# Kernel optimization log

Measured on AMD Instinct MI355X. Metric: run time of the kernel, lower is better.

Reference implementation:

```python
import jax, jax.numpy as jnp
import numpy as np

BN_EPS = 1e-5


def setup_inputs() -> dict:
    key = jax.random.key(0)
    ks = jax.random.split(key, 13)
    B, Ct, H, W = 2, 64, 32, 32
    Co, E = 32, 64
    Ho, Wo = 3 * H, 3 * W
    s = 0.05
    return {
        "x_thermal": jax.random.normal(ks[0], (B, Ct, H, W), jnp.float32),
        "x_optical": jax.random.normal(ks[1], (B, Co, Ho, Wo), jnp.float32),
        # 1x1 conv weights stored as [out_c, in_c]
        "q_w": jax.random.normal(ks[2], (E, Ct), jnp.float32) * s,
        "q_b": jax.random.normal(ks[3], (E,), jnp.float32) * s,
        "k_w": jax.random.normal(ks[4], (E, Co), jnp.float32) * s,
        "k_b": jax.random.normal(ks[5], (E,), jnp.float32) * s,
        "v_w": jax.random.normal(ks[6], (Co, Co), jnp.float32) * s,
        "v_b": jax.random.normal(ks[7], (Co,), jnp.float32) * s,
        # out ConvBlock: 1x1 conv (no bias) -> BatchNorm (eval, running stats) -> ReLU
        "out_w": jax.random.normal(ks[8], (Ct, Co), jnp.float32) * s,
        "bn_gamma": jnp.ones((Ct,), jnp.float32) + jax.random.normal(ks[9], (Ct,), jnp.float32) * 0.01,
        "bn_beta": jax.random.normal(ks[10], (Ct,), jnp.float32) * 0.01,
        "bn_mean": jax.random.normal(ks[11], (Ct,), jnp.float32) * 0.01,
        "bn_var": jax.random.uniform(ks[12], (Ct,), jnp.float32, 0.5, 1.5),
    }


def reference(x_thermal, x_optical, q_w, q_b, k_w, k_b, v_w, v_b,
              out_w, bn_gamma, bn_beta, bn_mean, bn_var):
    B, Co, Ho, Wo = x_optical.shape
    N = Ho * Wo
    # F.interpolate(mode='bilinear', align_corners=False) == jax.image.resize 'bilinear' (half-pixel)
    x_up = jax.image.resize(x_thermal, (B, x_thermal.shape[1], Ho, Wo), method="bilinear")
    # 1x1 conv projections
    q = (jnp.einsum("bchw,ec->behw", x_up, q_w) + q_b[None, :, None, None]).reshape(B, -1, N)
    k = (jnp.einsum("bchw,ec->behw", x_optical, k_w) + k_b[None, :, None, None]).reshape(B, -1, N)
    v = (jnp.einsum("bchw,oc->bohw", x_optical, v_w) + v_b[None, :, None, None]).reshape(B, -1, N)
    E = q.shape[1]
    # attn[b, n, m] = sum_e q[b,e,n] * k[b,e,m]  (full N x N score matrix)
    scores = jnp.einsum("ben,bem->bnm", q, k) / jnp.sqrt(jnp.asarray(E, q.dtype))
    attn = jax.nn.softmax(scores, axis=-1)
    # out = v @ attn^T : out[b,o,n] = sum_m v[b,o,m] * attn[b,n,m]
    out = jnp.einsum("bom,bnm->bon", v, attn).reshape(B, Co, Ho, Wo)
    # out ConvBlock: 1x1 conv (bias=False) -> BatchNorm (eval) -> ReLU
    g = jnp.einsum("bchw,tc->bthw", out, out_w)
    g = (g - bn_mean[None, :, None, None]) * (bn_gamma / jnp.sqrt(bn_var + BN_EPS))[None, :, None, None] \
        + bn_beta[None, :, None, None]
    return jax.nn.relu(g)
```

## Files before the change

kernel.cpp:

```cpp
#include <hip/hip_runtime.h>
#include <hip/hip_bf16.h>


constexpr int B   = 2;
constexpr int N   = 9216;
constexpr int E   = 64;
constexpr int CO  = 32;
constexpr int CT  = 64;
constexpr int KVBLK = 64;

constexpr int KP_BLK = 288;
constexpr int VP_BLK = 288;
constexpr int QP_BLK = 32;

typedef _Float16 f16x8 __attribute__((ext_vector_type(8)));
typedef _Float16 f16x4 __attribute__((ext_vector_type(4)));
typedef float    f32x4 __attribute__((ext_vector_type(4)));
typedef unsigned int u32;

#define MFMA(a, b, c) __builtin_amdgcn_mfma_f32_16x16x32_f16((a), (b), (c), 0, 0, 0)

#define GLOAD16(gsrc, ldst)                                                     \
  __builtin_amdgcn_global_load_lds(                                             \
      (const __attribute__((address_space(1))) u32*)(gsrc),                     \
      (__attribute__((address_space(3))) u32*)(ldst), 16, 0, 0)

#define SC 0.18033688011112042f

__global__ __launch_bounds__(256) void proj_fused_kernel(
    const float* __restrict__ xo,
    const float* __restrict__ kw, const float* __restrict__ kb,
    const float* __restrict__ vw, const float* __restrict__ vb,
    _Float16* __restrict__ K, _Float16* __restrict__ Vt,
    const float* __restrict__ xt,
    const float* __restrict__ qw, const float* __restrict__ qb,
    float* __restrict__ Qs)
{
  const int bid = blockIdx.x;
  if (bid < KP_BLK) {
    const int p      = (bid >> 2) * 256 + threadIdx.x;
    const int estart = (bid & 3) * 16;
    const int b = p / N, n = p % N;

    const float* xb = xo + (size_t)b * CO * N + n;
    float x[32];
#pragma unroll
    for (int c = 0; c < 32; ++c) x[c] = xb[(size_t)c * N];

    _Float16* Kp = K + (size_t)p * E + estart;
#pragma unroll 1
    for (int e0 = 0; e0 < 16; e0 += 8) {
      union { _Float16 h[8]; uint4 v; } pk;
#pragma unroll
      for (int j = 0; j < 8; ++j) {
        const int e = estart + e0 + j;
        float acc = kb[e];
#pragma unroll
        for (int c = 0; c < 32; ++c) acc += x[c] * kw[e * 32 + c];
        pk.h[j] = (_Float16)acc;
      }
      *(uint4*)(Kp + e0) = pk.v;
    }
  } else if (bid < KP_BLK + VP_BLK) {
    const int vbid   = bid - KP_BLK;
    const int p      = (vbid >> 2) * 256 + threadIdx.x;
    const int ostart = (vbid & 3) * 8;
    const int b = p / N, n = p % N;

    const float* xb = xo + (size_t)b * CO * N + n;
    float x[32];
#pragma unroll
    for (int c = 0; c < 32; ++c) x[c] = xb[(size_t)c * N];

    _Float16* Vp = Vt + (size_t)b * CO * N + n;
#pragma unroll 1
    for (int j = 0; j < 8; ++j) {
      const int o = ostart + j;
      float acc = vb[o];
#pragma unroll
      for (int c = 0; c < 32; ++c) acc += x[c] * vw[o * 32 + c];
      Vp[(size_t)o * N] = (_Float16)acc;
    }
  } else {
    const int qbid   = bid - KP_BLK - VP_BLK;
    const int pix    = (qbid >> 2) * 256 + threadIdx.x;
    const int estart = (qbid & 3) * 16;
    const int b = pix >> 10, p10 = pix & 1023;

    const float* xb = xt + (size_t)b * 64 * 1024 + p10;
    float x[64];
#pragma unroll
    for (int c = 0; c < 64; ++c) x[c] = xb[(size_t)c * 1024];

    float* Qp = Qs + (size_t)pix * 64 + estart;
#pragma unroll 1
    for (int e0 = 0; e0 < 16; e0 += 4) {
      f32x4 v;
#pragma unroll
      for (int j = 0; j < 4; ++j) {
        const int e = estart + e0 + j;
        float acc = qb[e];
#pragma unroll
        for (int c = 0; c < 64; ++c) acc += x[c] * qw[e * 64 + c];
        v[j] = acc * SC;
      }
      *(f32x4*)(Qp + e0) = v;
    }
  }
}

__global__ __launch_bounds__(256) void upsample_q_kernel(
    const float* __restrict__ Qs,
    _Float16* __restrict__ Q)
{
  const int tid = blockIdx.x * 256 + threadIdx.x;
  const int p   = tid >> 2;
  const int eq  = tid & 3;
  const int b   = p / N, n = p % N;
  const int ho  = n / 96, wo = n % 96;

  const float sh = (ho + 0.5f) * (1.0f / 3.0f) - 0.5f;
  const float sw = (wo + 0.5f) * (1.0f / 3.0f) - 0.5f;
  int h0 = (int)floorf(sh); const float fh = sh - (float)h0;
  int w0 = (int)floorf(sw); const float fw = sw - (float)w0;
  int h1 = min(h0 + 1, 31); h0 = max(h0, 0);
  int w1 = min(w0 + 1, 31); w0 = max(w0, 0);

  const float c00 = (1.f - fh) * (1.f - fw), c01 = (1.f - fh) * fw;
  const float c10 = fh * (1.f - fw),         c11 = fh * fw;

  const float* Qb = Qs + (size_t)b * 1024 * 64 + eq * 16;
  const f32x4* q00 = (const f32x4*)(Qb + (h0 * 32 + w0) * 64);
  const f32x4* q01 = (const f32x4*)(Qb + (h0 * 32 + w1) * 64);
  const f32x4* q10 = (const f32x4*)(Qb + (h1 * 32 + w0) * 64);
  const f32x4* q11 = (const f32x4*)(Qb + (h1 * 32 + w1) * 64);

  union { _Float16 h[16]; uint4 v[2]; } pk;
#pragma unroll
  for (int j4 = 0; j4 < 4; ++j4) {
    const f32x4 a = q00[j4] * c00 + q01[j4] * c01 + q10[j4] * c10 + q11[j4] * c11;
#pragma unroll
    for (int i = 0; i < 4; ++i) pk.h[4 * j4 + i] = (_Float16)a[i];
  }

  _Float16* Qp = Q + (size_t)p * E + eq * 16;
  *(uint4*)(Qp)     = pk.v[0];
  *(uint4*)(Qp + 8) = pk.v[1];
}

template<int SPLIT>
__global__ __launch_bounds__(256) void attn_kernel(
    const _Float16* __restrict__ Q,
    const _Float16* __restrict__ K,
    const _Float16* __restrict__ Vt,
    _Float16* __restrict__ OutWS,
    float* __restrict__ SumWS)
{
  constexpr int MCHUNK = N / SPLIT;
  constexpr int ROUNDS = MCHUNK / KVBLK;

  __shared__ _Float16 Kl[2][KVBLK][64];
  __shared__ _Float16 Vl[2][CO][KVBLK];

  const int tid  = threadIdx.x;
  const int wave = tid >> 6, lane = tid & 63;
  const int r16  = lane & 15, g = lane >> 4;

  const int work  = blockIdx.x;
  const int chunk = work & (SPLIT - 1);
  const int t128  = work / SPLIT;
  const int b     = t128 / 72;
  const int rowbase = (t128 % 72) * 128 + wave * 32;

  const _Float16* Qb = Q  + ((size_t)b * N + rowbase) * E;
  const _Float16* Kb = K  + (size_t)b * N * E;
  const _Float16* Vb = Vt + (size_t)b * CO * N;

  const int sub = lane >> 3, c8 = lane & 7;
  const int swz = 8 * (c8 ^ sub);

  const int mstart = chunk * MCHUNK;

  f16x8 qf[2][2];
#pragma unroll
  for (int rt = 0; rt < 2; ++rt)
#pragma unroll
    for (int ks = 0; ks < 2; ++ks)
      qf[rt][ks] = *(const f16x8*)(Qb + (rt * 16 + r16) * E + ks * 32 + g * 8);

  f16x8 onesf;
#pragma unroll
  for (int i = 0; i < 8; ++i) onesf[i] = (_Float16)1.0f;

  {
    const _Float16* gk = Kb + (size_t)(mstart + 16 * wave + sub) * E + swz;
    GLOAD16(gk,         &Kl[0][16 * wave][0]);
    GLOAD16(gk + 8 * E, &Kl[0][16 * wave + 8][0]);
    const _Float16* gv = Vb + (size_t)(8 * wave + sub) * N + mstart + swz;
    GLOAD16(gv,         &Vl[0][8 * wave][0]);
  }

  f32x4 oacc[2][2];
#pragma unroll
  for (int a = 0; a < 2; ++a)
#pragma unroll
    for (int c = 0; c < 2; ++c) oacc[a][c] = (f32x4){0.f, 0.f, 0.f, 0.f};
  f32x4 sacc[2];
  sacc[0] = (f32x4){0.f, 0.f, 0.f, 0.f};
  sacc[1] = (f32x4){0.f, 0.f, 0.f, 0.f};

  const int rsw   = (r16 & 7) << 4;
  const int kcol0 = ((0 * 64 + g * 16) ^ rsw) >> 1;
  const int kcol1 = ((1 * 64 + g * 16) ^ rsw) >> 1;

  __syncthreads();

  int cur = 0;
  for (int r = 0; r < ROUNDS; ++r) {
    if (r + 1 < ROUNDS) {
      const int m0 = mstart + (r + 1) * KVBLK;
      const _Float16* gk = Kb + (size_t)(m0 + 16 * wave + sub) * E + swz;
      GLOAD16(gk,         &Kl[cur ^ 1][16 * wave][0]);
      GLOAD16(gk + 8 * E, &Kl[cur ^ 1][16 * wave + 8][0]);
      const _Float16* gv = Vb + (size_t)(8 * wave + sub) * N + m0 + swz;
      GLOAD16(gv,         &Vl[cur ^ 1][8 * wave][0]);
    }

#pragma unroll
    for (int it = 0; it < 2; ++it) {
      f16x8 kf[2][2];
#pragma unroll
      for (int mt = 0; mt < 2; ++mt) {
        const int krow = it * 32 + mt * 16 + r16;
        kf[mt][0] = *(const f16x8*)&Kl[cur][krow][kcol0];
        kf[mt][1] = *(const f16x8*)&Kl[cur][krow][kcol1];
      }
      union { f16x4 h[2]; f16x8 v; } vf[2];
#pragma unroll
      for (int ot = 0; ot < 2; ++ot) {
        const int vrow = ot * 16 + r16;
        const int v0 = ((it * 64 + 8 * g) ^ rsw) >> 1;
        const int v1 = ((it * 64 + 32 + 8 * g) ^ rsw) >> 1;
        vf[ot].h[0] = *(const f16x4*)&Vl[cur][vrow][v0];
        vf[ot].h[1] = *(const f16x4*)&Vl[cur][vrow][v1];
      }

#pragma unroll
      for (int rt = 0; rt < 2; ++rt) {
        f32x4 s0 = (f32x4){0.f, 0.f, 0.f, 0.f};
        f32x4 s1 = (f32x4){0.f, 0.f, 0.f, 0.f};
        s0 = MFMA(kf[0][0], qf[rt][0], s0);
        s0 = MFMA(kf[0][1], qf[rt][1], s0);
        s1 = MFMA(kf[1][0], qf[rt][0], s1);
        s1 = MFMA(kf[1][1], qf[rt][1], s1);

        float p0[4], p1[4];
#pragma unroll
        for (int i = 0; i < 4; ++i) {
          p0[i] = __builtin_amdgcn_exp2f(s0[i]);
          p1[i] = __builtin_amdgcn_exp2f(s1[i]);
        }

        union { unsigned u[4]; f16x8 v; } pb;
        pb.u[0] = __builtin_bit_cast(unsigned, __builtin_amdgcn_cvt_pkrtz(p0[0], p0[1]));
        pb.u[1] = __builtin_bit_cast(unsigned, __builtin_amdgcn_cvt_pkrtz(p0[2], p0[3]));
        pb.u[2] = __builtin_bit_cast(unsigned, __builtin_amdgcn_cvt_pkrtz(p1[0], p1[1]));
        pb.u[3] = __builtin_bit_cast(unsigned, __builtin_amdgcn_cvt_pkrtz(p1[2], p1[3]));

        oacc[rt][0] = MFMA(vf[0].v, pb.v, oacc[rt][0]);
        oacc[rt][1] = MFMA(vf[1].v, pb.v, oacc[rt][1]);
        sacc[rt]    = MFMA(onesf,   pb.v, sacc[rt]);
      }
    }

    __syncthreads();
    cur ^= 1;
  }

  _Float16* OW = OutWS + (size_t)(chunk * B + b) * N * CO;
  float*    SW = SumWS + (size_t)(chunk * B + b) * N;
#pragma unroll
  for (int rt = 0; rt < 2; ++rt) {
    const int n = rowbase + rt * 16 + r16;
    if (g == 0) SW[n] = sacc[rt][0];
#pragma unroll
    for (int ot = 0; ot < 2; ++ot) {
      uint2 pko;
      pko.x = __builtin_bit_cast(unsigned,
                __builtin_amdgcn_cvt_pkrtz(oacc[rt][ot][0], oacc[rt][ot][1]));
      pko.y = __builtin_bit_cast(unsigned,
                __builtin_amdgcn_cvt_pkrtz(oacc[rt][ot][2], oacc[rt][ot][3]));
      *(uint2*)(OW + (size_t)n * CO + ot * 16 + 4 * g) = pko;
    }
  }
}

template<int SPLIT>
__global__ __launch_bounds__(256) void epi_kernel(
    const _Float16* __restrict__ OutWS, const float* __restrict__ SumWS,
    const float* __restrict__ ow, const float* __restrict__ gamma,
    const float* __restrict__ beta, const float* __restrict__ mean,
    const float* __restrict__ var, float* __restrict__ out)
{
  __shared__ float part[4][64][33];
  __shared__ float psum[4][64];

  const int tid  = threadIdx.x;
  const int nloc = tid & 63, grp = tid >> 6;
  const int pix  = blockIdx.x * 64 + nloc;
  const int b    = pix / N, n = pix % N;

  float accf[32];
#pragma unroll
  for (int j = 0; j < 32; ++j) accf[j] = 0.f;
  float ssum = 0.f;
#pragma unroll
  for (int k = 0; k < SPLIT / 4; ++k) {
    const int sc = grp * (SPLIT / 4) + k;
    const f16x8* src = (const f16x8*)(OutWS + ((size_t)(sc * B + b) * N + n) * CO);
#pragma unroll
    for (int j = 0; j < 4; ++j) {
      const f16x8 c = src[j];
#pragma unroll
      for (int i = 0; i < 8; ++i) accf[j * 8 + i] += (float)c[i];
    }
    ssum += SumWS[(size_t)(sc * B + b) * N + n];
  }
#pragma unroll
  for (int j = 0; j < 32; ++j) part[grp][nloc][j] = accf[j];
  psum[grp][nloc] = ssum;
  __syncthreads();

  const float s = psum[0][nloc] + psum[1][nloc] + psum[2][nloc] + psum[3][nloc];
  const float inv = 1.f / s;
  float onr[CO];
#pragma unroll
  for (int o = 0; o < CO; ++o)
    onr[o] = (part[0][nloc][o] + part[1][nloc][o] +
              part[2][nloc][o] + part[3][nloc][o]) * inv;

#pragma unroll
  for (int i = 0; i < 16; ++i) {
    const int t = grp + 4 * i;
    float acc2 = 0.f;
#pragma unroll
    for (int o = 0; o < CO; ++o) acc2 += onr[o] * ow[t * CO + o];
    const float scl = gamma[t] * rsqrtf(var[t] + 1e-5f);
    const float bia = beta[t] - mean[t] * scl;
    const float gv  = acc2 * scl + bia;
    out[(size_t)(b * CT + t) * N + n] = fmaxf(gv, 0.f);
  }
}

extern "C" void kernel_launch(void* const* d_in, const int* in_sizes, int n_in,
                              void* d_out, int out_size, void* d_ws, size_t ws_size,
                              hipStream_t stream) {
  const float* xt = (const float*)d_in[0];
  const float* xo = (const float*)d_in[1];
  const float* qw = (const float*)d_in[2];
  const float* qb = (const float*)d_in[3];
  const float* kw = (const float*)d_in[4];
  const float* kb = (const float*)d_in[5];
  const float* vw = (const float*)d_in[6];
  const float* vb = (const float*)d_in[7];
  const float* ow = (const float*)d_in[8];
  const float* gm = (const float*)d_in[9];
  const float* bt = (const float*)d_in[10];
  const float* mn = (const float*)d_in[11];
  const float* vr = (const float*)d_in[12];

  char* ws = (char*)d_ws;
  _Float16* Qd  = (_Float16*)ws;  ws += (size_t)B * N * E * 2;
  _Float16* Kd  = (_Float16*)ws;  ws += (size_t)B * N * E * 2;
  _Float16* Vtd = (_Float16*)ws;  ws += (size_t)B * CO * N * 2;
  float* Qs     = (float*)ws;     ws += (size_t)B * 1024 * 64 * 4;
  _Float16* OutWS = (_Float16*)ws;
  const size_t base   = (size_t)(ws - (char*)d_ws);
  const size_t need16 = base + (size_t)16 * B * N * (CO * 2 + 4);

  proj_fused_kernel<<<KP_BLK + VP_BLK + QP_BLK, 256, 0, stream>>>(
      xo, kw, kb, vw, vb, Kd, Vtd, xt, qw, qb, Qs);
  upsample_q_kernel<<<(B * N * 4) / 256, 256, 0, stream>>>(Qs, Qd);

  if (ws_size >= need16) {
    float* SumWS = (float*)(OutWS + (size_t)16 * B * N * CO);
    attn_kernel<16><<<(N / 128) * B * 16, 256, 0, stream>>>(Qd, Kd, Vtd, OutWS, SumWS);
    epi_kernel<16><<<(B * N) / 64, 256, 0, stream>>>(OutWS, SumWS, ow, gm, bt, mn, vr,
                                                     (float*)d_out);
  } else {
    float* SumWS = (float*)(OutWS + (size_t)8 * B * N * CO);
    attn_kernel<8><<<(N / 128) * B * 8, 256, 0, stream>>>(Qd, Kd, Vtd, OutWS, SumWS);
    epi_kernel<8><<<(B * N) / 64, 256, 0, stream>>>(OutWS, SumWS, ow, gm, bt, mn, vr,
                                                    (float*)d_out);
  }
}
```

Baseline: 158.8 us.

## Rewrite Q/K/V projections as MFMA GEMMs with swizzled LDS staging

Replaces the per-thread scalar FMA projection kernel with an MFMA-based GEMM. Each block stages 128 pixels of input in LDS as packed fp16 with an XOR swizzle, and computes K and V together so the optical input is read once instead of twice. Weights are converted to fp16 fragments on the fly. Inputs and weights now enter the projection at fp16 precision instead of fp32, which adds rounding error to Q, K and V.

```diff
diff --git a/kernel.cpp b/kernel.cpp
--- a/kernel.cpp
+++ b/kernel.cpp
@@ -9,9 +9,8 @@
 constexpr int CT  = 64;
 constexpr int KVBLK = 64;
 
-constexpr int KP_BLK = 288;
-constexpr int VP_BLK = 288;
-constexpr int QP_BLK = 32;
+constexpr int KV_BLKS = (B * N) / 128;
+constexpr int QS_BLKS = (B * 1024) / 128;
 
 typedef _Float16 f16x8 __attribute__((ext_vector_type(8)));
 typedef _Float16 f16x4 __attribute__((ext_vector_type(4)));
@@ -25,9 +24,11 @@
       (const __attribute__((address_space(1))) u32*)(gsrc),                     \
       (__attribute__((address_space(3))) u32*)(ldst), 16, 0, 0)
 
+#define PKRTZ(a, b) __builtin_bit_cast(unsigned, __builtin_amdgcn_cvt_pkrtz((a), (b)))
+
 #define SC 0.18033688011112042f
 
-__global__ __launch_bounds__(256) void proj_fused_kernel(
+__global__ __launch_bounds__(256) void proj_gemm_kernel(
     const float* __restrict__ xo,
     const float* __restrict__ kw, const float* __restrict__ kb,
     const float* __restrict__ vw, const float* __restrict__ vb,
@@ -36,75 +37,140 @@
     const float* __restrict__ qw, const float* __restrict__ qb,
     float* __restrict__ Qs)
 {
-  const int bid = blockIdx.x;
-  if (bid < KP_BLK) {
-    const int p      = (bid >> 2) * 256 + threadIdx.x;
-    const int estart = (bid & 3) * 16;
-    const int b = p / N, n = p % N;
-
-    const float* xb = xo + (size_t)b * CO * N + n;
-    float x[32];
-#pragma unroll
-    for (int c = 0; c < 32; ++c) x[c] = xb[(size_t)c * N];
-
-    _Float16* Kp = K + (size_t)p * E + estart;
-#pragma unroll 1
-    for (int e0 = 0; e0 < 16; e0 += 8) {
-      union { _Float16 h[8]; uint4 v; } pk;
-#pragma unroll
-      for (int j = 0; j < 8; ++j) {
-        const int e = estart + e0 + j;
-        float acc = kb[e];
-#pragma unroll
-        for (int c = 0; c < 32; ++c) acc += x[c] * kw[e * 32 + c];
-        pk.h[j] = (_Float16)acc;
-      }
-      *(uint4*)(Kp + e0) = pk.v;
-    }
-  } else if (bid < KP_BLK + VP_BLK) {
-    const int vbid   = bid - KP_BLK;
-    const int p      = (vbid >> 2) * 256 + threadIdx.x;
-    const int ostart = (vbid & 3) * 8;
-    const int b = p / N, n = p % N;
-
-    const float* xb = xo + (size_t)b * CO * N + n;
-    float x[32];
-#pragma unroll
-    for (int c = 0; c < 32; ++c) x[c] = xb[(size_t)c * N];
-
-    _Float16* Vp = Vt + (size_t)b * CO * N + n;
-#pragma unroll 1
-    for (int j = 0; j < 8; ++j) {
-      const int o = ostart + j;
-      float acc = vb[o];
-#pragma unroll
-      for (int c = 0; c < 32; ++c) acc += x[c] * vw[o * 32 + c];
-      Vp[(size_t)o * N] = (_Float16)acc;
+  __shared__ u32 Xl[128 * 32];
+
+  const int tid  = threadIdx.x;
+  const int wave = tid >> 6, lane = tid & 63;
+  const int r16  = lane & 15, g = lane >> 4;
+  const int bid  = blockIdx.x;
+
+  if (bid < KV_BLKS) {
+    const int p0 = bid * 128;
+    const int b  = p0 / N, n0 = p0 % N;
+
+    {
+      const int p  = tid & 127;
+      const int ch = tid >> 7;
+#pragma unroll
+      for (int cc = 0; cc < 8; ++cc) {
+        const int c = cc * 4 + ch * 2;
+        const float x0 = xo[((size_t)b * CO + c) * N + n0 + p];
+        const float x1 = xo[((size_t)b * CO + c + 1) * N + n0 + p];
+        Xl[p * 16 + ((c >> 1) ^ (p & 15))] = PKRTZ(x0, x1);
+      }
+    }
+    __syncthreads();
+
+    f16x8 xb[2];
+#pragma unroll
+    for (int pt = 0; pt < 2; ++pt) {
+      const int p = (wave * 2 + pt) * 16 + r16;
+      union { u32 u[4]; f16x8 v; } fr;
+#pragma unroll
+      for (int j = 0; j < 4; ++j)
+        fr.u[j] = Xl[p * 16 + ((g * 4 + j) ^ r16)];
+      xb[pt] = fr.v;
+    }
+
+#pragma unroll
+    for (int et = 0; et < 4; ++et) {
+      const float* kwe = kw + (size_t)(et * 16 + r16) * 32 + g * 8;
+      const f32x4 w0 = *(const f32x4*)(kwe);
+      const f32x4 w1 = *(const f32x4*)(kwe + 4);
+      union { u32 u[4]; f16x8 v; } af;
+      af.u[0] = PKRTZ(w0[0], w0[1]); af.u[1] = PKRTZ(w0[2], w0[3]);
+      af.u[2] = PKRTZ(w1[0], w1[1]); af.u[3] = PKRTZ(w1[2], w1[3]);
+
+      const int e0 = et * 16 + 4 * g;
+      const float b0 = kb[e0], b1 = kb[e0 + 1], b2 = kb[e0 + 2], b3 = kb[e0 + 3];
+#pragma unroll
+      for (int pt = 0; pt < 2; ++pt) {
+        f32x4 d = (f32x4){0.f, 0.f, 0.f, 0.f};
+        d = MFMA(af.v, xb[pt], d);
+        const int p = p0 + (wave * 2 + pt) * 16 + r16;
+        uint2 pk;
+        pk.x = PKRTZ(d[0] + b0, d[1] + b1);
+        pk.y = PKRTZ(d[2] + b2, d[3] + b3);
+        *(uint2*)(K + (size_t)p * E + e0) = pk;
+      }
+    }
+
+#pragma unroll
+    for (int ot = 0; ot < 2; ++ot) {
+      const float* vwo = vw + (size_t)(ot * 16 + r16) * 32 + g * 8;
+      const f32x4 w0 = *(const f32x4*)(vwo);
+      const f32x4 w1 = *(const f32x4*)(vwo + 4);
+      union { u32 u[4]; f16x8 v; } af;
+      af.u[0] = PKRTZ(w0[0], w0[1]); af.u[1] = PKRTZ(w0[2], w0[3]);
+      af.u[2] = PKRTZ(w1[0], w1[1]); af.u[3] = PKRTZ(w1[2], w1[3]);
+
+      const int o0 = ot * 16 + 4 * g;
+      const float b0 = vb[o0], b1 = vb[o0 + 1], b2 = vb[o0 + 2], b3 = vb[o0 + 3];
+#pragma unroll
+      for (int pt = 0; pt < 2; ++pt) {
+        f32x4 d = (f32x4){0.f, 0.f, 0.f, 0.f};
+        d = MFMA(af.v, xb[pt], d);
+        const int n = n0 + (wave * 2 + pt) * 16 + r16;
+        Vt[((size_t)b * CO + o0)     * N + n] = (_Float16)(d[0] + b0);
+        Vt[((size_t)b * CO + o0 + 1) * N + n] = (_Float16)(d[1] + b1);
+        Vt[((size_t)b * CO + o0 + 2) * N + n] = (_Float16)(d[2] + b2);
+        Vt[((size_t)b * CO + o0 + 3) * N + n] = (_Float16)(d[3] + b3);
+      }
     }
   } else {
-    const int qbid   = bid - KP_BLK - VP_BLK;
-    const int pix    = (qbid >> 2) * 256 + threadIdx.x;
-    const int estart = (qbid & 3) * 16;
-    const int b = pix >> 10, p10 = pix & 1023;
-
-    const float* xb = xt + (size_t)b * 64 * 1024 + p10;
-    float x[64];
-#pragma unroll
-    for (int c = 0; c < 64; ++c) x[c] = xb[(size_t)c * 1024];
-
-    float* Qp = Qs + (size_t)pix * 64 + estart;
-#pragma unroll 1
-    for (int e0 = 0; e0 < 16; e0 += 4) {
-      f32x4 v;
-#pragma unroll
-      for (int j = 0; j < 4; ++j) {
-        const int e = estart + e0 + j;
-        float acc = qb[e];
-#pragma unroll
-        for (int c = 0; c < 64; ++c) acc += x[c] * qw[e * 64 + c];
-        v[j] = acc * SC;
-      }
-      *(f32x4*)(Qp + e0) = v;
+    const int qbid = bid - KV_BLKS;
+    const int qp0  = qbid * 128;
+    const int b    = qp0 >> 10, p10 = qp0 & 1023;
+
+    {
+      const int p  = tid & 127;
+      const int ch = tid >> 7;
+#pragma unroll
+      for (int cc = 0; cc < 16; ++cc) {
+        const int c = cc * 4 + ch * 2;
+        const float x0 = xt[(((size_t)b * 64 + c) << 10) + p10 + p];
+        const float x1 = xt[(((size_t)b * 64 + c + 1) << 10) + p10 + p];
+        Xl[p * 32 + ((c >> 1) ^ (p & 31))] = PKRTZ(x0, x1);
+      }
+    }
+    __syncthreads();
+
+    f16x8 xb[2][2];
+#pragma unroll
+    for (int pt = 0; pt < 2; ++pt) {
+      const int pl = (wave * 2 + pt) * 16 + r16;
+#pragma unroll
+      for (int ks = 0; ks < 2; ++ks) {
+        union { u32 u[4]; f16x8 v; } fr;
+#pragma unroll
+        for (int j = 0; j < 4; ++j)
+          fr.u[j] = Xl[pl * 32 + ((ks * 16 + g * 4 + j) ^ (pl & 31))];
+        xb[pt][ks] = fr.v;
+      }
+    }
+
+#pragma unroll
+    for (int et = 0; et < 4; ++et) {
+      union { u32 u[4]; f16x8 v; } af[2];
+#pragma unroll
+      for (int ks = 0; ks < 2; ++ks) {
+        const float* qwe = qw + (size_t)(et * 16 + r16) * 64 + ks * 32 + g * 8;
+        const f32x4 w0 = *(const f32x4*)(qwe);
+        const f32x4 w1 = *(const f32x4*)(qwe + 4);
+        af[ks].u[0] = PKRTZ(w0[0], w0[1]); af[ks].u[1] = PKRTZ(w0[2], w0[3]);
+        af[ks].u[2] = PKRTZ(w1[0], w1[1]); af[ks].u[3] = PKRTZ(w1[2], w1[3]);
+      }
+
+      const int e0 = et * 16 + 4 * g;
+      const f32x4 qb4 = {qb[e0], qb[e0 + 1], qb[e0 + 2], qb[e0 + 3]};
+#pragma unroll
+      for (int pt = 0; pt < 2; ++pt) {
+        f32x4 d = (f32x4){0.f, 0.f, 0.f, 0.f};
+        d = MFMA(af[0].v, xb[pt][0], d);
+        d = MFMA(af[1].v, xb[pt][1], d);
+        const int pix = qp0 + (wave * 2 + pt) * 16 + r16;
+        *(f32x4*)(Qs + (size_t)pix * 64 + e0) = (d + qb4) * SC;
+      }
     }
   }
 }
@@ -262,10 +328,10 @@
         }
 
         union { unsigned u[4]; f16x8 v; } pb;
-        pb.u[0] = __builtin_bit_cast(unsigned, __builtin_amdgcn_cvt_pkrtz(p0[0], p0[1]));
-        pb.u[1] = __builtin_bit_cast(unsigned, __builtin_amdgcn_cvt_pkrtz(p0[2], p0[3]));
-        pb.u[2] = __builtin_bit_cast(unsigned, __builtin_amdgcn_cvt_pkrtz(p1[0], p1[1]));
-        pb.u[3] = __builtin_bit_cast(unsigned, __builtin_amdgcn_cvt_pkrtz(p1[2], p1[3]));
+        pb.u[0] = PKRTZ(p0[0], p0[1]);
+        pb.u[1] = PKRTZ(p0[2], p0[3]);
+        pb.u[2] = PKRTZ(p1[0], p1[1]);
+        pb.u[3] = PKRTZ(p1[2], p1[3]);
 
         oacc[rt][0] = MFMA(vf[0].v, pb.v, oacc[rt][0]);
         oacc[rt][1] = MFMA(vf[1].v, pb.v, oacc[rt][1]);
@@ -286,10 +352,8 @@
 #pragma unroll
     for (int ot = 0; ot < 2; ++ot) {
       uint2 pko;
-      pko.x = __builtin_bit_cast(unsigned,
-                __builtin_amdgcn_cvt_pkrtz(oacc[rt][ot][0], oacc[rt][ot][1]));
-      pko.y = __builtin_bit_cast(unsigned,
-                __builtin_amdgcn_cvt_pkrtz(oacc[rt][ot][2], oacc[rt][ot][3]));
+      pko.x = PKRTZ(oacc[rt][ot][0], oacc[rt][ot][1]);
+      pko.y = PKRTZ(oacc[rt][ot][2], oacc[rt][ot][3]);
       *(uint2*)(OW + (size_t)n * CO + ot * 16 + 4 * g) = pko;
     }
   }
@@ -378,7 +442,7 @@
   const size_t base   = (size_t)(ws - (char*)d_ws);
   const size_t need16 = base + (size_t)16 * B * N * (CO * 2 + 4);
 
-  proj_fused_kernel<<<KP_BLK + VP_BLK + QP_BLK, 256, 0, stream>>>(
+  proj_gemm_kernel<<<KV_BLKS + QS_BLKS, 256, 0, stream>>>(
       xo, kw, kb, vw, vb, Kd, Vtd, xt, qw, qb, Qs);
   upsample_q_kernel<<<(B * N * 4) / 256, 256, 0, stream>>>(Qs, Qd);
 
```

New measurement: 146.2 us. -7.9%, faster.
